# Optimization experiments

Hardware: AMD Instinct MI355X
Metric: run time of the kernel (lower is better)

Reference implementation:

```python
import jax, jax.numpy as jnp
import numpy as np

N = 50000      # num nodes
E = 1_200_000  # num edges
NID = 92       # node_input_dim
ED = 1         # edge_input_dim
H = 64         # hidden_dim
L = 5          # num_layers
EMB = 64       # embedding_dim
G = 256        # num graphs in batch
EPS = 1e-5


def _glorot(key, shape):
    fan_in, fan_out = shape[-2], shape[-1]
    lim = float(np.sqrt(6.0 / (fan_in + fan_out)))
    return jax.random.uniform(key, shape, jnp.float32, -lim, lim)


def setup_inputs() -> dict:
    key = jax.random.key(0)
    ks = jax.random.split(key, 16)
    inp = {
        "x": jax.random.normal(ks[0], (N, NID), jnp.float32),
        "edge_attr": jax.random.uniform(ks[1], (E, ED), jnp.float32),
        "edge_index": jax.random.randint(ks[2], (2, E), 0, N, jnp.int32),
        "batch": jnp.sort(jax.random.randint(ks[3], (N,), 0, G, jnp.int32)),
        # node embedding
        "node_W": _glorot(ks[4], (NID, H)),
        "node_b": jnp.zeros((H,), jnp.float32),
        # per-layer message net: Linear(2H+ED,H) -> BN -> SiLU -> Linear(H,H)
        "msg_W1": _glorot(ks[5], (L, 2 * H + ED, H)),
        "msg_b1": jnp.zeros((L, H), jnp.float32),
        "msg_g1": jnp.ones((L, H), jnp.float32),
        "msg_be1": jnp.zeros((L, H), jnp.float32),
        "msg_W2": _glorot(ks[6], (L, H, H)),
        "msg_b2": jnp.zeros((L, H), jnp.float32),
        # per-layer update net: Linear(2H,H) -> BN -> SiLU
        "upd_W": _glorot(ks[7], (L, 2 * H, H)),
        "upd_b": jnp.zeros((L, H), jnp.float32),
        "upd_g": jnp.ones((L, H), jnp.float32),
        "upd_be": jnp.zeros((L, H), jnp.float32),
        # output projection
        "out_W": _glorot(ks[8], (H, EMB)),
        "out_b": jnp.zeros((EMB,), jnp.float32),
    }
    return inp


def _bn(z, g, b):
    # BatchNorm1d, training-mode batch statistics (biased variance), eps=1e-5
    mu = jnp.mean(z, axis=0)
    var = jnp.var(z, axis=0)
    return (z - mu) * jax.lax.rsqrt(var + EPS) * g + b


def reference(x, edge_attr, node_W, node_b, msg_W1, msg_b1, msg_g1, msg_be1,
              msg_W2, msg_b2, upd_W, upd_b, upd_g, upd_be, out_W, out_b,
              edge_index, batch):
    src, dst = edge_index[0], edge_index[1]  # PyG: x_j = x[src], x_i = x[dst]
    h = x @ node_W + node_b                  # [N, H]
    deg = jax.ops.segment_sum(jnp.ones((E,), h.dtype), dst, num_segments=N)
    deg = jnp.maximum(deg, 1.0)[:, None]     # mean aggregation denominator
    for l in range(L):
        # message: cat([x_i, x_j, edge_attr]) -> Linear -> BN -> SiLU -> Linear
        m = jnp.concatenate([h[dst], h[src], edge_attr], axis=1)  # [E, 2H+ED]
        m = _bn(m @ msg_W1[l] + msg_b1[l], msg_g1[l], msg_be1[l])
        m = jax.nn.silu(m) @ msg_W2[l] + msg_b2[l]                # [E, H]
        # aggregate: scatter-mean to destination nodes
        agg = jax.ops.segment_sum(m, dst, num_segments=N) / deg   # [N, H]
        # update: cat([x, agg]) -> Linear -> BN -> SiLU
        u = jnp.concatenate([h, agg], axis=1) @ upd_W[l] + upd_b[l]
        h = jax.nn.silu(_bn(u, upd_g[l], upd_be[l]))              # [N, H]
    # global mean pool over graphs
    cnt = jnp.maximum(jax.ops.segment_sum(jnp.ones((N,), h.dtype), batch, num_segments=G), 1.0)
    g = jax.ops.segment_sum(h, batch, num_segments=G) / cnt[:, None]  # [G, H]
    return jax.nn.silu(g @ out_W + out_b)                              # [G, EMB]
```

## Files before the change

kernel.cpp:

```cpp
#include <hip/hip_runtime.h>
#include <hip/hip_bf16.h>

#define NN 50000
#define EE 1200000
#define GG 256
#define LL 5

__device__ __forceinline__ float silu_f(float x) {
    return x * __builtin_amdgcn_rcpf(1.0f + __expf(-x));
}
__device__ __forceinline__ int rfl(int x) { return __builtin_amdgcn_readfirstlane(x); }

__global__ __launch_bounds__(256) void k_hist(const int* __restrict__ ei, int* __restrict__ fill, int E) {
    int e = blockIdx.x * 256 + threadIdx.x;
    if (e < E) atomicAdd(&fill[ei[E + e]], 1);
}

__global__ __launch_bounds__(1024) void k_scan(const int* __restrict__ cnt, int* __restrict__ rowptr,
                                               float* __restrict__ degf, int* __restrict__ fill, int n) {
    __shared__ int wsum[16];
    __shared__ int carry_s;
    int tid = threadIdx.x, lane = tid & 63, wid = tid >> 6;
    if (tid == 0) carry_s = 0;
    __syncthreads();
    for (int base = 0; base < n; base += 1024) {
        int i = base + tid;
        int v = (i < n) ? cnt[i] : 0;
        int x = v;
        #pragma unroll
        for (int off = 1; off < 64; off <<= 1) {
            int t = __shfl_up(x, off);
            if (lane >= off) x += t;
        }
        if (lane == 63) wsum[wid] = x;
        __syncthreads();
        if (wid == 0 && lane < 16) {
            int w = wsum[lane];
            #pragma unroll
            for (int off = 1; off < 16; off <<= 1) {
                int t = __shfl_up(w, off);
                if (lane >= off) w += t;
            }
            wsum[lane] = w;
        }
        __syncthreads();
        int waveoff = (wid == 0) ? 0 : wsum[wid - 1];
        int inc = x + waveoff;
        int c = carry_s;
        int chunk_total = wsum[15];
        __syncthreads();
        if (i < n) {
            rowptr[i + 1] = c + inc;
            degf[i] = (float)(v > 0 ? v : 1);
            fill[i] = 0;
        }
        if (tid == 0) {
            if (base == 0) rowptr[0] = 0;
            carry_s = c + chunk_total;
        }
        __syncthreads();
    }
}

__global__ __launch_bounds__(256) void k_scatter(const int* __restrict__ ei, const float* __restrict__ ea,
                                                 const int* __restrict__ rowptr, int* __restrict__ fill,
                                                 unsigned int* __restrict__ edata, int E) {
    int e = blockIdx.x * 256 + threadIdx.x;
    if (e < E) {
        int d = ei[E + e];
        int pos = atomicAdd(&fill[d], 1);
        int idx = rowptr[d] + pos;
        int ea15 = (int)(ea[e] * 32768.0f + 0.5f);
        if (ea15 > 32767) ea15 = 32767;
        edata[idx] = ((unsigned int)ea15 << 17) | (unsigned int)ei[e];
    }
}

__global__ __launch_bounds__(256) void k_fold(const float* __restrict__ msg_W2, const float* __restrict__ msg_b2,
                                              const float* __restrict__ upd_W, float* __restrict__ W2p,
                                              float* __restrict__ b2p) {
    int l = blockIdx.x;
    const float* W2 = msg_W2 + (size_t)l * 4096;
    const float* U2 = upd_W + (size_t)l * 8192 + 4096;
    int lane = threadIdx.x & 63, wid = threadIdx.x >> 6;
    for (int ii = 0; ii < 16; ii++) {
        int i = rfl(wid * 16 + ii);
        float acc = 0.0f;
        for (int k = 0; k < 64; k++) acc = fmaf(W2[i * 64 + k], U2[k * 64 + lane], acc);
        W2p[(size_t)l * 4096 + i * 64 + lane] = acc;
    }
    if (wid == 0) {
        float acc = 0.0f;
        for (int k = 0; k < 64; k++) acc = fmaf(msg_b2[l * 64 + k], U2[k * 64 + lane], acc);
        b2p[l * 64 + lane] = acc;
    }
}

__global__ __launch_bounds__(256) void k_node_emb(const float* __restrict__ x, const float* __restrict__ W,
                                                  const float* __restrict__ b, float* __restrict__ h, int n) {
    __shared__ float sW[92 * 64];
    for (int i = threadIdx.x; i < 92 * 64; i += 256) sW[i] = W[i];
    __syncthreads();
    int lane = threadIdx.x & 63;
    int gw = (blockIdx.x * 256 + threadIdx.x) >> 6;
    int nw = (gridDim.x * 256) >> 6;
    float bj = b[lane];
    int tiles = n >> 3;
    for (int t = gw; t < tiles; t += nw) {
        int rb = rfl(t << 3);
        float acc[8];
        #pragma unroll
        for (int r = 0; r < 8; r++) acc[r] = bj;
        for (int kb = 0; kb < 80; kb += 16) {
            float wv[16];
            #pragma unroll
            for (int t2 = 0; t2 < 16; t2++) wv[t2] = sW[(kb + t2) * 64 + lane];
            #pragma unroll
            for (int r = 0; r < 8; r++) {
                const float* xr = x + (size_t)(rb + r) * 92 + kb;
                #pragma unroll
                for (int t2 = 0; t2 < 16; t2++) acc[r] = fmaf(xr[t2], wv[t2], acc[r]);
            }
        }
        {
            float wv[12];
            #pragma unroll
            for (int t2 = 0; t2 < 12; t2++) wv[t2] = sW[(80 + t2) * 64 + lane];
            #pragma unroll
            for (int r = 0; r < 8; r++) {
                const float* xr = x + (size_t)(rb + r) * 92 + 80;
                #pragma unroll
                for (int t2 = 0; t2 < 12; t2++) acc[r] = fmaf(xr[t2], wv[t2], acc[r]);
            }
        }
        #pragma unroll
        for (int r = 0; r < 8; r++) h[(size_t)(rb + r) * 64 + lane] = acc[r];
    }
}

__global__ __launch_bounds__(256) void k_node_pre(const float* __restrict__ h, const float* __restrict__ W1,
                                                  const float* __restrict__ b1, float* __restrict__ Hd,
                                                  _Float16* __restrict__ Hs, int n) {
    __shared__ float sA[4096], sB[4096];
    for (int i = threadIdx.x; i < 4096; i += 256) { sA[i] = W1[i]; sB[i] = W1[4096 + i]; }
    __syncthreads();
    int lane = threadIdx.x & 63;
    int gw = (blockIdx.x * 256 + threadIdx.x) >> 6;
    int nw = (gridDim.x * 256) >> 6;
    float bj = b1[lane];
    int tiles = n >> 3;
    for (int t = gw; t < tiles; t += nw) {
        int rb = rfl(t << 3);
        float accA[8], accB[8];
        #pragma unroll
        for (int r = 0; r < 8; r++) { accA[r] = bj; accB[r] = 0.0f; }
        for (int kb = 0; kb < 64; kb += 16) {
            float wA[16], wB[16];
            #pragma unroll
            for (int t2 = 0; t2 < 16; t2++) { wA[t2] = sA[(kb + t2) * 64 + lane]; wB[t2] = sB[(kb + t2) * 64 + lane]; }
            #pragma unroll
            for (int r = 0; r < 8; r++) {
                const float* hr = h + (size_t)(rb + r) * 64 + kb;
                #pragma unroll
                for (int t2 = 0; t2 < 16; t2++) {
                    float hk = hr[t2];
                    accA[r] = fmaf(hk, wA[t2], accA[r]);
                    accB[r] = fmaf(hk, wB[t2], accB[r]);
                }
            }
        }
        #pragma unroll
        for (int r = 0; r < 8; r++) {
            Hd[(size_t)(rb + r) * 64 + lane] = accA[r];
            Hs[(size_t)(rb + r) * 64 + lane] = (_Float16)accB[r];
        }
    }
}

__global__ __launch_bounds__(256) void k_edge_stats(const float* __restrict__ Hd, const _Float16* __restrict__ Hs,
                                                    const int* __restrict__ rowptr, const unsigned int* __restrict__ edata,
                                                    const float* __restrict__ w1e,
                                                    float* __restrict__ esum, float* __restrict__ esq, int n) {
    __shared__ float rs[4][64], rq[4][64];
    int wid = threadIdx.x >> 6, lane = threadIdx.x & 63;
    int gw = (blockIdx.x * 256 + threadIdx.x) >> 6;
    int nw = (gridDim.x * 256) >> 6;
    float wj = w1e[lane] * (1.0f / 32768.0f);
    float s = 0.0f, q = 0.0f;
    for (int node = gw; node < n; node += nw) {
        int nu = rfl(node);
        int e0 = rowptr[nu], e1 = rowptr[nu + 1];
        if (e0 == e1) continue;
        float hd = Hd[(size_t)nu * 64 + lane];
        int e = e0;
        for (; e + 8 <= e1; e += 8) {
            float hs[8], av[8];
            #pragma unroll
            for (int j = 0; j < 8; j++) {
                unsigned int p = edata[e + j];
                int sidx = rfl((int)(p & 0x1FFFFu));
                av[j] = (float)rfl((int)(p >> 17));
                hs[j] = (float)Hs[(size_t)sidx * 64 + lane];
            }
            #pragma unroll
            for (int j = 0; j < 8; j++) {
                float z = fmaf(av[j], wj, hd) + hs[j];
                s += z;
                q = fmaf(z, z, q);
            }
        }
        for (; e < e1; e++) {
            unsigned int p = edata[e];
            int sidx = rfl((int)(p & 0x1FFFFu));
            float a = (float)rfl((int)(p >> 17));
            float z = fmaf(a, wj, hd) + (float)Hs[(size_t)sidx * 64 + lane];
            s += z;
            q = fmaf(z, z, q);
        }
    }
    rs[wid][lane] = s; rq[wid][lane] = q;
    __syncthreads();
    if (wid == 0) {
        float ts = rs[0][lane] + rs[1][lane] + rs[2][lane] + rs[3][lane];
        float tq = rq[0][lane] + rq[1][lane] + rq[2][lane] + rq[3][lane];
        atomicAdd(&esum[lane], ts);
        atomicAdd(&esq[lane], tq);
    }
}

__global__ __launch_bounds__(256) void k_edge_agg(const float* __restrict__ Hd, const _Float16* __restrict__ Hs,
                                                  const int* __restrict__ rowptr, const unsigned int* __restrict__ edata,
                                                  const float* __restrict__ w1e,
                                                  const float* __restrict__ esum, const float* __restrict__ esq,
                                                  const float* __restrict__ g1, const float* __restrict__ be1,
                                                  const float* __restrict__ degf, float* __restrict__ sacc,
                                                  int n, float invE) {
    int lane = threadIdx.x & 63;
    float mean = esum[lane] * invE;
    float var = esq[lane] * invE - mean * mean;
    float inv = rsqrtf(var + 1e-5f);
    float sc = inv * g1[lane];
    float sh = fmaf(-mean, sc, be1[lane]);
    float wj = w1e[lane] * (1.0f / 32768.0f);
    int gw = (blockIdx.x * 256 + threadIdx.x) >> 6;
    int nw = (gridDim.x * 256) >> 6;
    for (int node = gw; node < n; node += nw) {
        int nu = rfl(node);
        int e0 = rowptr[nu], e1 = rowptr[nu + 1];
        float acc = 0.0f;
        float hd = Hd[(size_t)nu * 64 + lane];
        int e = e0;
        for (; e + 8 <= e1; e += 8) {
            float hs[8], av[8];
            #pragma unroll
            for (int j = 0; j < 8; j++) {
                unsigned int p = edata[e + j];
                int sidx = rfl((int)(p & 0x1FFFFu));
                av[j] = (float)rfl((int)(p >> 17));
                hs[j] = (float)Hs[(size_t)sidx * 64 + lane];
            }
            #pragma unroll
            for (int j = 0; j < 8; j++) {
                float z = fmaf(av[j], wj, hd) + hs[j];
                acc += silu_f(fmaf(z, sc, sh));
            }
        }
        for (; e < e1; e++) {
            unsigned int p = edata[e];
            int sidx = rfl((int)(p & 0x1FFFFu));
            float a = (float)rfl((int)(p >> 17));
            float z = fmaf(a, wj, hd) + (float)Hs[(size_t)sidx * 64 + lane];
            acc += silu_f(fmaf(z, sc, sh));
        }
        sacc[(size_t)nu * 64 + lane] = acc / degf[nu];
    }
}

__global__ __launch_bounds__(256) void k_node_upd(const float* __restrict__ h, const float* __restrict__ sacc,
                                                  const float* __restrict__ U1, const float* __restrict__ W2p,
                                                  const float* __restrict__ b2p, const float* __restrict__ ub,
                                                  const int* __restrict__ rowptr, float* __restrict__ u,
                                                  float* __restrict__ usum, float* __restrict__ usq, int n) {
    __shared__ float sU[4096], sP[4096];
    __shared__ float rs[4][64], rq[4][64];
    for (int i = threadIdx.x; i < 4096; i += 256) { sU[i] = U1[i]; sP[i] = W2p[i]; }
    __syncthreads();
    int wid = threadIdx.x >> 6, lane = threadIdx.x & 63;
    int gw = (blockIdx.x * 256 + threadIdx.x) >> 6;
    int nw = (gridDim.x * 256) >> 6;
    float b2j = b2p[lane], ubj = ub[lane];
    float s = 0.0f, q = 0.0f;
    int tiles = n >> 3;
    for (int t = gw; t < tiles; t += nw) {
        int rb = rfl(t << 3);
        float acc[8];
        #pragma unroll
        for (int r = 0; r < 8; r++) {
            int c0 = rowptr[rb + r], c1 = rowptr[rb + r + 1];
            acc[r] = ubj + (c1 > c0 ? b2j : 0.0f);
        }
        for (int kb = 0; kb < 64; kb += 16) {
            float wU[16], wP[16];
            #pragma unroll
            for (int t2 = 0; t2 < 16; t2++) { wU[t2] = sU[(kb + t2) * 64 + lane]; wP[t2] = sP[(kb + t2) * 64 + lane]; }
            #pragma unroll
            for (int r = 0; r < 8; r++) {
                const float* hr = h + (size_t)(rb + r) * 64 + kb;
                const float* sr = sacc + (size_t)(rb + r) * 64 + kb;
                #pragma unroll
                for (int t2 = 0; t2 < 16; t2++) {
                    acc[r] = fmaf(hr[t2], wU[t2], acc[r]);
                    acc[r] = fmaf(sr[t2], wP[t2], acc[r]);
                }
            }
        }
        #pragma unroll
        for (int r = 0; r < 8; r++) {
            u[(size_t)(rb + r) * 64 + lane] = acc[r];
            s += acc[r];
            q = fmaf(acc[r], acc[r], q);
        }
    }
    rs[wid][lane] = s; rq[wid][lane] = q;
    __syncthreads();
    if (wid == 0) {
        float ts = rs[0][lane] + rs[1][lane] + rs[2][lane] + rs[3][lane];
        float tq = rq[0][lane] + rq[1][lane] + rq[2][lane] + rq[3][lane];
        atomicAdd(&usum[lane], ts);
        atomicAdd(&usq[lane], tq);
    }
}

__global__ __launch_bounds__(256) void k_node_bn(const float* __restrict__ u, const float* __restrict__ usum,
                                                 const float* __restrict__ usq, const float* __restrict__ g,
                                                 const float* __restrict__ be, float* __restrict__ h,
                                                 int n, float invN) {
    __shared__ float ssc[64], ssh[64];
    if (threadIdx.x < 64) {
        int j = threadIdx.x;
        float mean = usum[j] * invN;
        float var = usq[j] * invN - mean * mean;
        float inv = rsqrtf(var + 1e-5f);
        float sc = inv * g[j];
        ssc[j] = sc;
        ssh[j] = fmaf(-mean, sc, be[j]);
    }
    __syncthreads();
    int total = n * 64;
    for (int i = blockIdx.x * 256 + threadIdx.x; i < total; i += gridDim.x * 256) {
        int j = i & 63;
        float y = fmaf(u[i], ssc[j], ssh[j]);
        h[i] = silu_f(y);
    }
}

__global__ __launch_bounds__(256) void k_bn_pool(const float* __restrict__ u, const float* __restrict__ usum,
                                                 const float* __restrict__ usq, const float* __restrict__ g,
                                                 const float* __restrict__ be, const int* __restrict__ batch,
                                                 float* __restrict__ gsum, float* __restrict__ gcnt,
                                                 int n, float invN) {
    __shared__ float ssc[64], ssh[64];
    if (threadIdx.x < 64) {
        int j = threadIdx.x;
        float mean = usum[j] * invN;
        float var = usq[j] * invN - mean * mean;
        float inv = rsqrtf(var + 1e-5f);
        float sc = inv * g[j];
        ssc[j] = sc;
        ssh[j] = fmaf(-mean, sc, be[j]);
    }
    __syncthreads();
    int lane = threadIdx.x & 63;
    int gw = (blockIdx.x * 256 + threadIdx.x) >> 6;
    int nw = (gridDim.x * 256) >> 6;
    int per = (n + nw - 1) / nw;
    int start = gw * per;
    int end = start + per; if (end > n) end = n;
    if (start >= end) return;
    float sc = ssc[lane], sh = ssh[lane];
    int cur = batch[start];
    float acc = 0.0f, c = 0.0f;
    for (int i = start; i < end; i++) {
        int b = batch[i];
        if (b != cur) {
            atomicAdd(&gsum[(size_t)cur * 64 + lane], acc);
            if (lane == 0) atomicAdd(&gcnt[cur], c);
            cur = b; acc = 0.0f; c = 0.0f;
        }
        float y = fmaf(u[(size_t)i * 64 + lane], sc, sh);
        acc += silu_f(y);
        c += 1.0f;
    }
    atomicAdd(&gsum[(size_t)cur * 64 + lane], acc);
    if (lane == 0) atomicAdd(&gcnt[cur], c);
}

__global__ __launch_bounds__(256) void k_out(const float* __restrict__ gsum, const float* __restrict__ gcnt,
                                             const float* __restrict__ OW, const float* __restrict__ ob,
                                             float* __restrict__ out, int G) {
    __shared__ float sW[4096];
    for (int i = threadIdx.x; i < 4096; i += 256) sW[i] = OW[i];
    __syncthreads();
    int lane = threadIdx.x & 63;
    int gw = (blockIdx.x * 256 + threadIdx.x) >> 6;
    int nw = (gridDim.x * 256) >> 6;
    for (int g = gw; g < G; g += nw) {
        int gu = rfl(g);
        float c = gcnt[gu]; if (c < 1.0f) c = 1.0f;
        float ci = 1.0f / c;
        float acc = ob[lane];
        const float* gr = gsum + (size_t)gu * 64;
        #pragma unroll
        for (int k = 0; k < 64; k++) acc = fmaf(gr[k] * ci, sW[k * 64 + lane], acc);
        out[(size_t)gu * 64 + lane] = silu_f(acc);
    }
}

extern "C" void kernel_launch(void* const* d_in, const int* in_sizes, int n_in,
                              void* d_out, int out_size, void* d_ws, size_t ws_size,
                              hipStream_t stream) {
    const int N = NN, E = EE, G = GG, L = LL;
    const float* x         = (const float*)d_in[0];
    const float* edge_attr = (const float*)d_in[1];
    const int*   edge_index= (const int*)d_in[2];
    const int*   batch     = (const int*)d_in[3];
    const float* node_W    = (const float*)d_in[4];
    const float* node_b    = (const float*)d_in[5];
    const float* msg_W1    = (const float*)d_in[6];
    const float* msg_b1    = (const float*)d_in[7];
    const float* msg_g1    = (const float*)d_in[8];
    const float* msg_be1   = (const float*)d_in[9];
    const float* msg_W2    = (const float*)d_in[10];
    const float* msg_b2    = (const float*)d_in[11];
    const float* upd_W     = (const float*)d_in[12];
    const float* upd_b     = (const float*)d_in[13];
    const float* upd_g     = (const float*)d_in[14];
    const float* upd_be    = (const float*)d_in[15];
    const float* out_W     = (const float*)d_in[16];
    const float* out_b     = (const float*)d_in[17];
    float* out = (float*)d_out;

    char* ws = (char*)d_ws;
    size_t off = 0;
    auto alloc = [&](size_t b) { size_t o = off; off = (off + b + 255) & ~(size_t)255; return o; };
    float* h    = (float*)(ws + alloc((size_t)N * 64 * 4));
    float* Hd   = (float*)(ws + alloc((size_t)N * 64 * 4));
    _Float16* Hs = (_Float16*)(ws + alloc((size_t)N * 64 * 2));
    float* sacc = (float*)(ws + alloc((size_t)N * 64 * 4));
    unsigned int* edata = (unsigned int*)(ws + alloc((size_t)E * 4));
    int* rowptr = (int*)  (ws + alloc((size_t)(N + 1) * 4));
    float* degf = (float*)(ws + alloc((size_t)N * 4));
    float* W2p  = (float*)(ws + alloc((size_t)L * 4096 * 4));
    float* b2p  = (float*)(ws + alloc((size_t)L * 64 * 4));
    size_t zero_begin = off;
    int*   fill = (int*)  (ws + alloc((size_t)N * 4));
    float* stats= (float*)(ws + alloc((size_t)L * 4 * 64 * 4));
    float* gsum = (float*)(ws + alloc((size_t)(G * 64 + G) * 4));
    size_t zero_end = off;
    float* gcnt = gsum + (size_t)G * 64;
    float* u = Hd;

    hipMemsetAsync(ws + zero_begin, 0, zero_end - zero_begin, stream);

    k_hist<<<(E + 255) / 256, 256, 0, stream>>>(edge_index, fill, E);
    k_scan<<<1, 1024, 0, stream>>>(fill, rowptr, degf, fill, N);
    k_scatter<<<(E + 255) / 256, 256, 0, stream>>>(edge_index, edge_attr, rowptr, fill, edata, E);

    k_fold<<<L, 256, 0, stream>>>(msg_W2, msg_b2, upd_W, W2p, b2p);
    k_node_emb<<<1024, 256, 0, stream>>>(x, node_W, node_b, h, N);

    for (int l = 0; l < L; l++) {
        const float* W1  = msg_W1 + (size_t)l * 129 * 64;
        const float* w1e = W1 + 128 * 64;
        float* esum = stats + (size_t)l * 256;
        float* esq  = esum + 64;
        float* usum = esum + 128;
        float* usq  = esum + 192;
        k_node_pre<<<1024, 256, 0, stream>>>(h, W1, msg_b1 + l * 64, Hd, Hs, N);
        k_edge_stats<<<2048, 256, 0, stream>>>(Hd, Hs, rowptr, edata, w1e, esum, esq, N);
        k_edge_agg<<<2048, 256, 0, stream>>>(Hd, Hs, rowptr, edata, w1e, esum, esq,
                                             msg_g1 + l * 64, msg_be1 + l * 64, degf, sacc, N, 1.0f / E);
        k_node_upd<<<1024, 256, 0, stream>>>(h, sacc, upd_W + (size_t)l * 8192, W2p + (size_t)l * 4096,
                                             b2p + (size_t)l * 64, upd_b + l * 64, rowptr,
                                             u, usum, usq, N);
        if (l < L - 1) {
            k_node_bn<<<2048, 256, 0, stream>>>(u, usum, usq, upd_g + l * 64, upd_be + l * 64, h, N, 1.0f / N);
        } else {
            k_bn_pool<<<256, 256, 0, stream>>>(u, usum, usq, upd_g + l * 64, upd_be + l * 64,
                                               batch, gsum, gcnt, N, 1.0f / N);
        }
    }

    k_out<<<64, 256, 0, stream>>>(gsum, gcnt, out_W, out_b, out, G);
}
```

Before: 1.358 ms.

## Fuse node BatchNorm+SiLU into consumer kernels and stage row tiles in LDS

Removes the standalone k_node_bn pass. The next layer's k_node_pre and k_node_upd now recompute BN scale/shift from the accumulated stats and apply BN+SiLU while loading the previous u tile. The node GEMM kernels (embedding, pre, update) switch from grid-stride warps reading rows from global memory to one block per 64- or 32-row tile. Each tile is copied into shared memory with float4 loads, and the FMAs use vectorized LDS reads. This saves a full N×64 read/write per layer and a kernel launch. The cost is BN+SiLU work repeated in two kernels, an extra u buffer, and larger shared-memory footprints that may reduce occupancy.

```diff
diff --git a/kernel.cpp b/kernel.cpp
--- a/kernel.cpp
+++ b/kernel.cpp
@@ -98,81 +98,144 @@
 
 __global__ __launch_bounds__(256) void k_node_emb(const float* __restrict__ x, const float* __restrict__ W,
                                                   const float* __restrict__ b, float* __restrict__ h, int n) {
-    __shared__ float sW[92 * 64];
-    for (int i = threadIdx.x; i < 92 * 64; i += 256) sW[i] = W[i];
-    __syncthreads();
-    int lane = threadIdx.x & 63;
-    int gw = (blockIdx.x * 256 + threadIdx.x) >> 6;
-    int nw = (gridDim.x * 256) >> 6;
+    __shared__ float sW[5888];
+    __shared__ float xt[5888];
+    int tid = threadIdx.x;
+    for (int i = tid; i < 5888; i += 256) sW[i] = W[i];
+    int rb = blockIdx.x << 6;
+    int valid = n - rb; if (valid > 64) valid = 64;
+    {
+        const float4* g4 = (const float4*)(x + (size_t)rb * 92);
+        float4* x4 = (float4*)xt;
+        int cnt4 = (valid * 92) >> 2;
+        for (int i = tid; i < cnt4; i += 256) x4[i] = g4[i];
+    }
+    __syncthreads();
+    int lane = tid & 63, wid = tid >> 6;
     float bj = b[lane];
-    int tiles = n >> 3;
-    for (int t = gw; t < tiles; t += nw) {
-        int rb = rfl(t << 3);
+    #pragma unroll
+    for (int g8 = 0; g8 < 2; g8++) {
+        int r0 = (wid << 4) + (g8 << 3);
+        if (rb + r0 >= n) continue;
         float acc[8];
         #pragma unroll
         for (int r = 0; r < 8; r++) acc[r] = bj;
         for (int kb = 0; kb < 80; kb += 16) {
             float wv[16];
             #pragma unroll
-            for (int t2 = 0; t2 < 16; t2++) wv[t2] = sW[(kb + t2) * 64 + lane];
+            for (int t = 0; t < 16; t++) wv[t] = sW[(kb + t) * 64 + lane];
             #pragma unroll
             for (int r = 0; r < 8; r++) {
-                const float* xr = x + (size_t)(rb + r) * 92 + kb;
+                const float4* xr = (const float4*)&xt[(r0 + r) * 92 + kb];
                 #pragma unroll
-                for (int t2 = 0; t2 < 16; t2++) acc[r] = fmaf(xr[t2], wv[t2], acc[r]);
+                for (int q = 0; q < 4; q++) {
+                    float4 v = xr[q];
+                    acc[r] = fmaf(v.x, wv[q * 4 + 0], acc[r]);
+                    acc[r] = fmaf(v.y, wv[q * 4 + 1], acc[r]);
+                    acc[r] = fmaf(v.z, wv[q * 4 + 2], acc[r]);
+                    acc[r] = fmaf(v.w, wv[q * 4 + 3], acc[r]);
+                }
             }
         }
         {
             float wv[12];
             #pragma unroll
-            for (int t2 = 0; t2 < 12; t2++) wv[t2] = sW[(80 + t2) * 64 + lane];
+            for (int t = 0; t < 12; t++) wv[t] = sW[(80 + t) * 64 + lane];
             #pragma unroll
             for (int r = 0; r < 8; r++) {
-                const float* xr = x + (size_t)(rb + r) * 92 + 80;
+                const float4* xr = (const float4*)&xt[(r0 + r) * 92 + 80];
                 #pragma unroll
-                for (int t2 = 0; t2 < 12; t2++) acc[r] = fmaf(xr[t2], wv[t2], acc[r]);
-            }
-        }
-        #pragma unroll
-        for (int r = 0; r < 8; r++) h[(size_t)(rb + r) * 64 + lane] = acc[r];
-    }
-}
-
-__global__ __launch_bounds__(256) void k_node_pre(const float* __restrict__ h, const float* __restrict__ W1,
-                                                  const float* __restrict__ b1, float* __restrict__ Hd,
-                                                  _Float16* __restrict__ Hs, int n) {
-    __shared__ float sA[4096], sB[4096];
-    for (int i = threadIdx.x; i < 4096; i += 256) { sA[i] = W1[i]; sB[i] = W1[4096 + i]; }
-    __syncthreads();
-    int lane = threadIdx.x & 63;
-    int gw = (blockIdx.x * 256 + threadIdx.x) >> 6;
-    int nw = (gridDim.x * 256) >> 6;
+                for (int q = 0; q < 3; q++) {
+                    float4 v = xr[q];
+                    acc[r] = fmaf(v.x, wv[q * 4 + 0], acc[r]);
+                    acc[r] = fmaf(v.y, wv[q * 4 + 1], acc[r]);
+                    acc[r] = fmaf(v.z, wv[q * 4 + 2], acc[r]);
+                    acc[r] = fmaf(v.w, wv[q * 4 + 3], acc[r]);
+                }
+            }
+        }
+        #pragma unroll
+        for (int r = 0; r < 8; r++) {
+            int grow = rb + r0 + r;
+            if (grow < n) h[(size_t)grow * 64 + lane] = acc[r];
+        }
+    }
+}
+
+__global__ __launch_bounds__(256) void k_node_pre(const float* src, int bn,
+        const float* __restrict__ bnsum, const float* __restrict__ bnsq,
+        const float* __restrict__ bng, const float* __restrict__ bnbe, float invN,
+        const float* __restrict__ W1, const float* __restrict__ b1,
+        float* __restrict__ Hd, _Float16* __restrict__ Hs, int n) {
+    __shared__ float sA[4096], sB[4096], xt[4096];
+    __shared__ float ssc[64], ssh[64];
+    int tid = threadIdx.x;
+    if (tid < 64) {
+        float sc = 1.0f, sh = 0.0f;
+        if (bn) {
+            float mean = bnsum[tid] * invN;
+            float var = bnsq[tid] * invN - mean * mean;
+            float inv = rsqrtf(var + 1e-5f);
+            sc = inv * bng[tid];
+            sh = fmaf(-mean, sc, bnbe[tid]);
+        }
+        ssc[tid] = sc; ssh[tid] = sh;
+    }
+    for (int i = tid; i < 4096; i += 256) { sA[i] = W1[i]; sB[i] = W1[4096 + i]; }
+    __syncthreads();
+    int rb = blockIdx.x << 6;
+    int valid = n - rb; if (valid > 64) valid = 64;
+    {
+        const float4* g4 = (const float4*)(src + (size_t)rb * 64);
+        float4* x4 = (float4*)xt;
+        int cnt4 = valid << 4;
+        for (int i = tid; i < cnt4; i += 256) {
+            float4 v = g4[i];
+            if (bn) {
+                int c = (i & 15) << 2;
+                v.x = silu_f(fmaf(v.x, ssc[c],     ssh[c]));
+                v.y = silu_f(fmaf(v.y, ssc[c + 1], ssh[c + 1]));
+                v.z = silu_f(fmaf(v.z, ssc[c + 2], ssh[c + 2]));
+                v.w = silu_f(fmaf(v.w, ssc[c + 3], ssh[c + 3]));
+            }
+            x4[i] = v;
+        }
+    }
+    __syncthreads();
+    int lane = tid & 63, wid = tid >> 6;
     float bj = b1[lane];
-    int tiles = n >> 3;
-    for (int t = gw; t < tiles; t += nw) {
-        int rb = rfl(t << 3);
+    #pragma unroll
+    for (int g8 = 0; g8 < 2; g8++) {
+        int r0 = (wid << 4) + (g8 << 3);
+        if (rb + r0 >= n) continue;
         float accA[8], accB[8];
         #pragma unroll
         for (int r = 0; r < 8; r++) { accA[r] = bj; accB[r] = 0.0f; }
+        #pragma unroll
         for (int kb = 0; kb < 64; kb += 16) {
             float wA[16], wB[16];
             #pragma unroll
-            for (int t2 = 0; t2 < 16; t2++) { wA[t2] = sA[(kb + t2) * 64 + lane]; wB[t2] = sB[(kb + t2) * 64 + lane]; }
+            for (int t = 0; t < 16; t++) { wA[t] = sA[(kb + t) * 64 + lane]; wB[t] = sB[(kb + t) * 64 + lane]; }
             #pragma unroll
             for (int r = 0; r < 8; r++) {
-                const float* hr = h + (size_t)(rb + r) * 64 + kb;
+                const float4* xr = (const float4*)&xt[(r0 + r) * 64 + kb];
                 #pragma unroll
-                for (int t2 = 0; t2 < 16; t2++) {
-                    float hk = hr[t2];
-                    accA[r] = fmaf(hk, wA[t2], accA[r]);
-                    accB[r] = fmaf(hk, wB[t2], accB[r]);
+                for (int q = 0; q < 4; q++) {
+                    float4 v = xr[q];
+                    accA[r] = fmaf(v.x, wA[q * 4 + 0], accA[r]); accB[r] = fmaf(v.x, wB[q * 4 + 0], accB[r]);
+                    accA[r] = fmaf(v.y, wA[q * 4 + 1], accA[r]); accB[r] = fmaf(v.y, wB[q * 4 + 1], accB[r]);
+                    accA[r] = fmaf(v.z, wA[q * 4 + 2], accA[r]); accB[r] = fmaf(v.z, wB[q * 4 + 2], accB[r]);
+                    accA[r] = fmaf(v.w, wA[q * 4 + 3], accA[r]); accB[r] = fmaf(v.w, wB[q * 4 + 3], accB[r]);
                 }
             }
         }
         #pragma unroll
         for (int r = 0; r < 8; r++) {
-            Hd[(size_t)(rb + r) * 64 + lane] = accA[r];
-            Hs[(size_t)(rb + r) * 64 + lane] = (_Float16)accB[r];
+            int grow = rb + r0 + r;
+            if (grow < n) {
+                Hd[(size_t)grow * 64 + lane] = accA[r];
+                Hs[(size_t)grow * 64 + lane] = (_Float16)accB[r];
+            }
         }
     }
 }
@@ -276,49 +339,95 @@
     }
 }
 
-__global__ __launch_bounds__(256) void k_node_upd(const float* __restrict__ h, const float* __restrict__ sacc,
-                                                  const float* __restrict__ U1, const float* __restrict__ W2p,
-                                                  const float* __restrict__ b2p, const float* __restrict__ ub,
-                                                  const int* __restrict__ rowptr, float* __restrict__ u,
-                                                  float* __restrict__ usum, float* __restrict__ usq, int n) {
-    __shared__ float sU[4096], sP[4096];
+__global__ __launch_bounds__(256) void k_node_upd(const float* src, int bn,
+        const float* __restrict__ bnsum, const float* __restrict__ bnsq,
+        const float* __restrict__ bng, const float* __restrict__ bnbe, float invN,
+        const float* __restrict__ sacc,
+        const float* __restrict__ U1, const float* __restrict__ W2p,
+        const float* __restrict__ b2p, const float* __restrict__ ub,
+        const int* __restrict__ rowptr, float* u,
+        float* __restrict__ usum, float* __restrict__ usq, int n) {
+    __shared__ float sU[4096], sP[4096], ht[2048], st[2048];
+    __shared__ float ssc[64], ssh[64];
     __shared__ float rs[4][64], rq[4][64];
-    for (int i = threadIdx.x; i < 4096; i += 256) { sU[i] = U1[i]; sP[i] = W2p[i]; }
-    __syncthreads();
-    int wid = threadIdx.x >> 6, lane = threadIdx.x & 63;
-    int gw = (blockIdx.x * 256 + threadIdx.x) >> 6;
-    int nw = (gridDim.x * 256) >> 6;
+    int tid = threadIdx.x;
+    if (tid < 64) {
+        float sc = 1.0f, sh = 0.0f;
+        if (bn) {
+            float mean = bnsum[tid] * invN;
+            float var = bnsq[tid] * invN - mean * mean;
+            float inv = rsqrtf(var + 1e-5f);
+            sc = inv * bng[tid];
+            sh = fmaf(-mean, sc, bnbe[tid]);
+        }
+        ssc[tid] = sc; ssh[tid] = sh;
+    }
+    for (int i = tid; i < 4096; i += 256) { sU[i] = U1[i]; sP[i] = W2p[i]; }
+    __syncthreads();
+    int rb = blockIdx.x << 5;
+    int valid = n - rb; if (valid > 32) valid = 32;
+    {
+        const float4* g4 = (const float4*)(src + (size_t)rb * 64);
+        const float4* s4 = (const float4*)(sacc + (size_t)rb * 64);
+        float4* h4 = (float4*)ht;
+        float4* t4 = (float4*)st;
+        int cnt4 = valid << 4;
+        for (int i = tid; i < cnt4; i += 256) {
+            float4 v = g4[i];
+            if (bn) {
+                int c = (i & 15) << 2;
+                v.x = silu_f(fmaf(v.x, ssc[c],     ssh[c]));
+                v.y = silu_f(fmaf(v.y, ssc[c + 1], ssh[c + 1]));
+                v.z = silu_f(fmaf(v.z, ssc[c + 2], ssh[c + 2]));
+                v.w = silu_f(fmaf(v.w, ssc[c + 3], ssh[c + 3]));
+            }
+            h4[i] = v;
+            t4[i] = s4[i];
+        }
+    }
+    __syncthreads();
+    int lane = tid & 63, wid = tid >> 6;
     float b2j = b2p[lane], ubj = ub[lane];
     float s = 0.0f, q = 0.0f;
-    int tiles = n >> 3;
-    for (int t = gw; t < tiles; t += nw) {
-        int rb = rfl(t << 3);
+    int r0 = wid << 3;
+    if (rb + r0 < n) {
         float acc[8];
         #pragma unroll
         for (int r = 0; r < 8; r++) {
-            int c0 = rowptr[rb + r], c1 = rowptr[rb + r + 1];
-            acc[r] = ubj + (c1 > c0 ? b2j : 0.0f);
-        }
+            int grow = rb + r0 + r;
+            if (grow < n) {
+                int c0 = rowptr[grow], c1 = rowptr[grow + 1];
+                acc[r] = ubj + (c1 > c0 ? b2j : 0.0f);
+            } else acc[r] = 0.0f;
+        }
+        #pragma unroll
         for (int kb = 0; kb < 64; kb += 16) {
             float wU[16], wP[16];
             #pragma unroll
-            for (int t2 = 0; t2 < 16; t2++) { wU[t2] = sU[(kb + t2) * 64 + lane]; wP[t2] = sP[(kb + t2) * 64 + lane]; }
+            for (int t = 0; t < 16; t++) { wU[t] = sU[(kb + t) * 64 + lane]; wP[t] = sP[(kb + t) * 64 + lane]; }
             #pragma unroll
             for (int r = 0; r < 8; r++) {
-                const float* hr = h + (size_t)(rb + r) * 64 + kb;
-                const float* sr = sacc + (size_t)(rb + r) * 64 + kb;
+                const float4* hr = (const float4*)&ht[(r0 + r) * 64 + kb];
+                const float4* sr = (const float4*)&st[(r0 + r) * 64 + kb];
                 #pragma unroll
-                for (int t2 = 0; t2 < 16; t2++) {
-                    acc[r] = fmaf(hr[t2], wU[t2], acc[r]);
-                    acc[r] = fmaf(sr[t2], wP[t2], acc[r]);
+                for (int qq = 0; qq < 4; qq++) {
+                    float4 hv = hr[qq];
+                    float4 sv = sr[qq];
+                    acc[r] = fmaf(hv.x, wU[qq * 4 + 0], acc[r]); acc[r] = fmaf(sv.x, wP[qq * 4 + 0], acc[r]);
+                    acc[r] = fmaf(hv.y, wU[qq * 4 + 1], acc[r]); acc[r] = fmaf(sv.y, wP[qq * 4 + 1], acc[r]);
+                    acc[r] = fmaf(hv.z, wU[qq * 4 + 2], acc[r]); acc[r] = fmaf(sv.z, wP[qq * 4 + 2], acc[r]);
+                    acc[r] = fmaf(hv.w, wU[qq * 4 + 3], acc[r]); acc[r] = fmaf(sv.w, wP[qq * 4 + 3], acc[r]);
                 }
             }
         }
         #pragma unroll
         for (int r = 0; r < 8; r++) {
-            u[(size_t)(rb + r) * 64 + lane] = acc[r];
-            s += acc[r];
-            q = fmaf(acc[r], acc[r], q);
+            int grow = rb + r0 + r;
+            if (grow < n) {
+                u[(size_t)grow * 64 + lane] = acc[r];
+                s += acc[r];
+                q = fmaf(acc[r], acc[r], q);
+            }
         }
     }
     rs[wid][lane] = s; rq[wid][lane] = q;
@@ -328,29 +437,6 @@
         float tq = rq[0][lane] + rq[1][lane] + rq[2][lane] + rq[3][lane];
         atomicAdd(&usum[lane], ts);
         atomicAdd(&usq[lane], tq);
-    }
-}
-
-__global__ __launch_bounds__(256) void k_node_bn(const float* __restrict__ u, const float* __restrict__ usum,
-                                                 const float* __restrict__ usq, const float* __restrict__ g,
-                                                 const float* __restrict__ be, float* __restrict__ h,
-                                                 int n, float invN) {
-    __shared__ float ssc[64], ssh[64];
-    if (threadIdx.x < 64) {
-        int j = threadIdx.x;
-        float mean = usum[j] * invN;
-        float var = usq[j] * invN - mean * mean;
-        float inv = rsqrtf(var + 1e-5f);
-        float sc = inv * g[j];
-        ssc[j] = sc;
-        ssh[j] = fmaf(-mean, sc, be[j]);
-    }
-    __syncthreads();
-    int total = n * 64;
-    for (int i = blockIdx.x * 256 + threadIdx.x; i < total; i += gridDim.x * 256) {
-        int j = i & 63;
-        float y = fmaf(u[i], ssc[j], ssh[j]);
-        h[i] = silu_f(y);
     }
 }
 
@@ -443,10 +529,11 @@
     char* ws = (char*)d_ws;
     size_t off = 0;
     auto alloc = [&](size_t b) { size_t o = off; off = (off + b + 255) & ~(size_t)255; return o; };
-    float* h    = (float*)(ws + alloc((size_t)N * 64 * 4));
+    float* h0   = (float*)(ws + alloc((size_t)N * 64 * 4));
     float* Hd   = (float*)(ws + alloc((size_t)N * 64 * 4));
     _Float16* Hs = (_Float16*)(ws + alloc((size_t)N * 64 * 2));
     float* sacc = (float*)(ws + alloc((size_t)N * 64 * 4));
+    float* u    = (float*)(ws + alloc((size_t)N * 64 * 4));
     unsigned int* edata = (unsigned int*)(ws + alloc((size_t)E * 4));
     int* rowptr = (int*)  (ws + alloc((size_t)(N + 1) * 4));
     float* degf = (float*)(ws + alloc((size_t)N * 4));
@@ -458,7 +545,6 @@
     float* gsum = (float*)(ws + alloc((size_t)(G * 64 + G) * 4));
     size_t zero_end = off;
     float* gcnt = gsum + (size_t)G * 64;
-    float* u = Hd;
 
     hipMemsetAsync(ws + zero_begin, 0, zero_end - zero_begin, stream);
 
@@ -467,7 +553,9 @@
     k_scatter<<<(E + 255) / 256, 256, 0, stream>>>(edge_index, edge_attr, rowptr, fill, edata, E);
 
     k_fold<<<L, 256, 0, stream>>>(msg_W2, msg_b2, upd_W, W2p, b2p);
-    k_node_emb<<<1024, 256, 0, stream>>>(x, node_W, node_b, h, N);
+    const int TILES64 = (N + 63) / 64;
+    const int TILES32 = (N + 31) / 32;
+    k_node_emb<<<TILES64, 256, 0, stream>>>(x, node_W, node_b, h0, N);
 
     for (int l = 0; l < L; l++) {
         const float* W1  = msg_W1 + (size_t)l * 129 * 64;
@@ -476,20 +564,23 @@
         float* esq  = esum + 64;
         float* usum = esum + 128;
         float* usq  = esum + 192;
-        k_node_pre<<<1024, 256, 0, stream>>>(h, W1, msg_b1 + l * 64, Hd, Hs, N);
+        int lp = (l > 0) ? (l - 1) : 0;
+        const float* src = (l == 0) ? h0 : u;
+        int bn = (l == 0) ? 0 : 1;
+        const float* psum = stats + (size_t)lp * 256 + 128;
+        const float* psq  = psum + 64;
+        k_node_pre<<<TILES64, 256, 0, stream>>>(src, bn, psum, psq, upd_g + lp * 64, upd_be + lp * 64,
+                                                1.0f / N, W1, msg_b1 + l * 64, Hd, Hs, N);
         k_edge_stats<<<2048, 256, 0, stream>>>(Hd, Hs, rowptr, edata, w1e, esum, esq, N);
         k_edge_agg<<<2048, 256, 0, stream>>>(Hd, Hs, rowptr, edata, w1e, esum, esq,
                                              msg_g1 + l * 64, msg_be1 + l * 64, degf, sacc, N, 1.0f / E);
-        k_node_upd<<<1024, 256, 0, stream>>>(h, sacc, upd_W + (size_t)l * 8192, W2p + (size_t)l * 4096,
-                                             b2p + (size_t)l * 64, upd_b + l * 64, rowptr,
-                                             u, usum, usq, N);
-        if (l < L - 1) {
-            k_node_bn<<<2048, 256, 0, stream>>>(u, usum, usq, upd_g + l * 64, upd_be + l * 64, h, N, 1.0f / N);
-        } else {
-            k_bn_pool<<<256, 256, 0, stream>>>(u, usum, usq, upd_g + l * 64, upd_be + l * 64,
-                                               batch, gsum, gcnt, N, 1.0f / N);
-        }
-    }
-
+        k_node_upd<<<TILES32, 256, 0, stream>>>(src, bn, psum, psq, upd_g + lp * 64, upd_be + lp * 64,
+                                                1.0f / N, sacc, upd_W + (size_t)l * 8192,
+                                                W2p + (size_t)l * 4096, b2p + (size_t)l * 64,
+                                                upd_b + l * 64, rowptr, u, usum, usq, N);
+    }
+
+    k_bn_pool<<<256, 256, 0, stream>>>(u, stats + 4 * 256 + 128, stats + 4 * 256 + 192,
+                                       upd_g + 4 * 64, upd_be + 4 * 64, batch, gsum, gcnt, N, 1.0f / N);
     k_out<<<64, 256, 0, stream>>>(gsum, gcnt, out_W, out_b, out, G);
 }
```

New measurement: 3.230 ms. 138% more time.

## Partition edges by source-node half for cache-friendly two-phase gathers

Applied to the files above, without the earlier changes.

Each destination's CSR segment is split into edges whose source lies in the lower half of the nodes and edges from the upper half. The edge stats and aggregation kernels now sweep all nodes twice, once per half, so the random Hs gather touches only half of the table at a time and has a better chance of staying in cache. Hd loads and sacc stores become nontemporal, and both edge kernels launch with 1024 blocks instead of 2048. The cost is an extra histogram counter and atomic pass in preprocessing, a second sweep over rowptr and Hd per kernel, and a read-modify-write of sacc in the aggregation kernel.

```diff
diff --git a/kernel.cpp b/kernel.cpp
--- a/kernel.cpp
+++ b/kernel.cpp
@@ -5,15 +5,21 @@
 #define EE 1200000
 #define GG 256
 #define LL 5
+#define NH 25000
 
 __device__ __forceinline__ float silu_f(float x) {
     return x * __builtin_amdgcn_rcpf(1.0f + __expf(-x));
 }
 __device__ __forceinline__ int rfl(int x) { return __builtin_amdgcn_readfirstlane(x); }
 
-__global__ __launch_bounds__(256) void k_hist(const int* __restrict__ ei, int* __restrict__ fill, int E) {
+__global__ __launch_bounds__(256) void k_hist(const int* __restrict__ ei, int* __restrict__ fill,
+                                              int* __restrict__ cntlo, int E) {
     int e = blockIdx.x * 256 + threadIdx.x;
-    if (e < E) atomicAdd(&fill[ei[E + e]], 1);
+    if (e < E) {
+        int d = ei[E + e];
+        atomicAdd(&fill[d], 1);
+        if (ei[e] < NH) atomicAdd(&cntlo[d], 1);
+    }
 }
 
 __global__ __launch_bounds__(1024) void k_scan(const int* __restrict__ cnt, int* __restrict__ rowptr,
@@ -63,16 +69,25 @@
 }
 
 __global__ __launch_bounds__(256) void k_scatter(const int* __restrict__ ei, const float* __restrict__ ea,
-                                                 const int* __restrict__ rowptr, int* __restrict__ fill,
+                                                 const int* __restrict__ rowptr, const int* __restrict__ cntlo,
+                                                 int* __restrict__ fill_lo, int* __restrict__ fill_hi,
                                                  unsigned int* __restrict__ edata, int E) {
     int e = blockIdx.x * 256 + threadIdx.x;
     if (e < E) {
         int d = ei[E + e];
-        int pos = atomicAdd(&fill[d], 1);
-        int idx = rowptr[d] + pos;
+        int s = ei[e];
+        int idx;
+        if (s < NH) {
+            int pos = atomicAdd(&fill_lo[d], 1);
+            idx = rowptr[d] + pos;
+        } else {
+            int pos = atomicAdd(&fill_hi[d], 1);
+            idx = rowptr[d] + cntlo[d] + pos;
+        }
         int ea15 = (int)(ea[e] * 32768.0f + 0.5f);
         if (ea15 > 32767) ea15 = 32767;
-        edata[idx] = ((unsigned int)ea15 << 17) | (unsigned int)ei[e];
+        unsigned int v = ((unsigned int)ea15 << 17) | (unsigned int)s;
+        __builtin_nontemporal_store(v, &edata[idx]);
     }
 }
 
@@ -178,7 +193,8 @@
 }
 
 __global__ __launch_bounds__(256) void k_edge_stats(const float* __restrict__ Hd, const _Float16* __restrict__ Hs,
-                                                    const int* __restrict__ rowptr, const unsigned int* __restrict__ edata,
+                                                    const int* __restrict__ rowptr, const int* __restrict__ cntlo,
+                                                    const unsigned int* __restrict__ edata,
                                                     const float* __restrict__ w1e,
                                                     float* __restrict__ esum, float* __restrict__ esq, int n) {
     __shared__ float rs[4][64], rq[4][64];
@@ -187,35 +203,40 @@
     int nw = (gridDim.x * 256) >> 6;
     float wj = w1e[lane] * (1.0f / 32768.0f);
     float s = 0.0f, q = 0.0f;
-    for (int node = gw; node < n; node += nw) {
-        int nu = rfl(node);
-        int e0 = rowptr[nu], e1 = rowptr[nu + 1];
-        if (e0 == e1) continue;
-        float hd = Hd[(size_t)nu * 64 + lane];
-        int e = e0;
-        for (; e + 8 <= e1; e += 8) {
-            float hs[8], av[8];
-            #pragma unroll
-            for (int j = 0; j < 8; j++) {
-                unsigned int p = edata[e + j];
+    for (int phase = 0; phase < 2; phase++) {
+        for (int node = gw; node < n; node += nw) {
+            int nu = rfl(node);
+            int r0 = rowptr[nu], r1 = rowptr[nu + 1];
+            int mid = r0 + cntlo[nu];
+            int e0 = phase ? mid : r0;
+            int e1 = phase ? r1 : mid;
+            if (e0 >= e1) continue;
+            float hd = __builtin_nontemporal_load(Hd + (size_t)nu * 64 + lane);
+            int e = e0;
+            for (; e + 8 <= e1; e += 8) {
+                float hs[8], av[8];
+                #pragma unroll
+                for (int j = 0; j < 8; j++) {
+                    unsigned int p = edata[e + j];
+                    int sidx = rfl((int)(p & 0x1FFFFu));
+                    av[j] = (float)rfl((int)(p >> 17));
+                    hs[j] = (float)Hs[(size_t)sidx * 64 + lane];
+                }
+                #pragma unroll
+                for (int j = 0; j < 8; j++) {
+                    float z = fmaf(av[j], wj, hd) + hs[j];
+                    s += z;
+                    q = fmaf(z, z, q);
+                }
+            }
+            for (; e < e1; e++) {
+                unsigned int p = edata[e];
                 int sidx = rfl((int)(p & 0x1FFFFu));
-                av[j] = (float)rfl((int)(p >> 17));
-                hs[j] = (float)Hs[(size_t)sidx * 64 + lane];
-            }
-            #pragma unroll
-            for (int j = 0; j < 8; j++) {
-                float z = fmaf(av[j], wj, hd) + hs[j];
+                float a = (float)rfl((int)(p >> 17));
+                float z = fmaf(a, wj, hd) + (float)Hs[(size_t)sidx * 64 + lane];
                 s += z;
                 q = fmaf(z, z, q);
             }
-        }
-        for (; e < e1; e++) {
-            unsigned int p = edata[e];
-            int sidx = rfl((int)(p & 0x1FFFFu));
-            float a = (float)rfl((int)(p >> 17));
-            float z = fmaf(a, wj, hd) + (float)Hs[(size_t)sidx * 64 + lane];
-            s += z;
-            q = fmaf(z, z, q);
         }
     }
     rs[wid][lane] = s; rq[wid][lane] = q;
@@ -229,7 +250,8 @@
 }
 
 __global__ __launch_bounds__(256) void k_edge_agg(const float* __restrict__ Hd, const _Float16* __restrict__ Hs,
-                                                  const int* __restrict__ rowptr, const unsigned int* __restrict__ edata,
+                                                  const int* __restrict__ rowptr, const int* __restrict__ cntlo,
+                                                  const unsigned int* __restrict__ edata,
                                                   const float* __restrict__ w1e,
                                                   const float* __restrict__ esum, const float* __restrict__ esq,
                                                   const float* __restrict__ g1, const float* __restrict__ be1,
@@ -244,35 +266,46 @@
     float wj = w1e[lane] * (1.0f / 32768.0f);
     int gw = (blockIdx.x * 256 + threadIdx.x) >> 6;
     int nw = (gridDim.x * 256) >> 6;
-    for (int node = gw; node < n; node += nw) {
-        int nu = rfl(node);
-        int e0 = rowptr[nu], e1 = rowptr[nu + 1];
-        float acc = 0.0f;
-        float hd = Hd[(size_t)nu * 64 + lane];
-        int e = e0;
-        for (; e + 8 <= e1; e += 8) {
-            float hs[8], av[8];
-            #pragma unroll
-            for (int j = 0; j < 8; j++) {
-                unsigned int p = edata[e + j];
+    for (int phase = 0; phase < 2; phase++) {
+        for (int node = gw; node < n; node += nw) {
+            int nu = rfl(node);
+            int r0 = rowptr[nu], r1 = rowptr[nu + 1];
+            int mid = r0 + cntlo[nu];
+            int e0 = phase ? mid : r0;
+            int e1 = phase ? r1 : mid;
+            float acc = 0.0f;
+            float hd = __builtin_nontemporal_load(Hd + (size_t)nu * 64 + lane);
+            int e = e0;
+            for (; e + 8 <= e1; e += 8) {
+                float hs[8], av[8];
+                #pragma unroll
+                for (int j = 0; j < 8; j++) {
+                    unsigned int p = edata[e + j];
+                    int sidx = rfl((int)(p & 0x1FFFFu));
+                    av[j] = (float)rfl((int)(p >> 17));
+                    hs[j] = (float)Hs[(size_t)sidx * 64 + lane];
+                }
+                #pragma unroll
+                for (int j = 0; j < 8; j++) {
+                    float z = fmaf(av[j], wj, hd) + hs[j];
+                    acc += silu_f(fmaf(z, sc, sh));
+                }
+            }
+            for (; e < e1; e++) {
+                unsigned int p = edata[e];
                 int sidx = rfl((int)(p & 0x1FFFFu));
-                av[j] = (float)rfl((int)(p >> 17));
-                hs[j] = (float)Hs[(size_t)sidx * 64 + lane];
-            }
-            #pragma unroll
-            for (int j = 0; j < 8; j++) {
-                float z = fmaf(av[j], wj, hd) + hs[j];
+                float a = (float)rfl((int)(p >> 17));
+                float z = fmaf(a, wj, hd) + (float)Hs[(size_t)sidx * 64 + lane];
                 acc += silu_f(fmaf(z, sc, sh));
             }
-        }
-        for (; e < e1; e++) {
-            unsigned int p = edata[e];
-            int sidx = rfl((int)(p & 0x1FFFFu));
-            float a = (float)rfl((int)(p >> 17));
-            float z = fmaf(a, wj, hd) + (float)Hs[(size_t)sidx * 64 + lane];
-            acc += silu_f(fmaf(z, sc, sh));
-        }
-        sacc[(size_t)nu * 64 + lane] = acc / degf[nu];
+            float* sp = sacc + (size_t)nu * 64 + lane;
+            if (phase == 0) {
+                __builtin_nontemporal_store(acc, sp);
+            } else {
+                float prev = *sp;
+                __builtin_nontemporal_store((prev + acc) / degf[nu], sp);
+            }
+        }
     }
 }
 
@@ -454,6 +487,8 @@
     float* b2p  = (float*)(ws + alloc((size_t)L * 64 * 4));
     size_t zero_begin = off;
     int*   fill = (int*)  (ws + alloc((size_t)N * 4));
+    int*   cntlo= (int*)  (ws + alloc((size_t)N * 4));
+    int*   fillh= (int*)  (ws + alloc((size_t)N * 4));
     float* stats= (float*)(ws + alloc((size_t)L * 4 * 64 * 4));
     float* gsum = (float*)(ws + alloc((size_t)(G * 64 + G) * 4));
     size_t zero_end = off;
@@ -462,9 +497,9 @@
 
     hipMemsetAsync(ws + zero_begin, 0, zero_end - zero_begin, stream);
 
-    k_hist<<<(E + 255) / 256, 256, 0, stream>>>(edge_index, fill, E);
+    k_hist<<<(E + 255) / 256, 256, 0, stream>>>(edge_index, fill, cntlo, E);
     k_scan<<<1, 1024, 0, stream>>>(fill, rowptr, degf, fill, N);
-    k_scatter<<<(E + 255) / 256, 256, 0, stream>>>(edge_index, edge_attr, rowptr, fill, edata, E);
+    k_scatter<<<(E + 255) / 256, 256, 0, stream>>>(edge_index, edge_attr, rowptr, cntlo, fill, fillh, edata, E);
 
     k_fold<<<L, 256, 0, stream>>>(msg_W2, msg_b2, upd_W, W2p, b2p);
     k_node_emb<<<1024, 256, 0, stream>>>(x, node_W, node_b, h, N);
@@ -477,8 +512,8 @@
         float* usum = esum + 128;
         float* usq  = esum + 192;
         k_node_pre<<<1024, 256, 0, stream>>>(h, W1, msg_b1 + l * 64, Hd, Hs, N);
-        k_edge_stats<<<2048, 256, 0, stream>>>(Hd, Hs, rowptr, edata, w1e, esum, esq, N);
-        k_edge_agg<<<2048, 256, 0, stream>>>(Hd, Hs, rowptr, edata, w1e, esum, esq,
+        k_edge_stats<<<1024, 256, 0, stream>>>(Hd, Hs, rowptr, cntlo, edata, w1e, esum, esq, N);
+        k_edge_agg<<<1024, 256, 0, stream>>>(Hd, Hs, rowptr, cntlo, edata, w1e, esum, esq,
                                              msg_g1 + l * 64, msg_be1 + l * 64, degf, sacc, N, 1.0f / E);
         k_node_upd<<<1024, 256, 0, stream>>>(h, sacc, upd_W + (size_t)l * 8192, W2p + (size_t)l * 4096,
                                              b2p + (size_t)l * 64, upd_b + l * 64, rowptr,
```

Measured after the change: 1.618 ms. 1.19x slower.
